# Kernel optimization log

Hardware: AMD Instinct MI355X
Metric: run time of the kernel (lower is better)

The kernel has to match this reference:

```python
import jax, jax.numpy as jnp
import numpy as np
from jax import lax

B, LEN_SEQ, D_MODEL, N_HEAD, FACTOR, D_FF = 16, 512, 512, 8, 5, 2048
EPS = 1e-5


def layer_norm(x):
    mu = x.mean(-1, keepdims=True)
    var = ((x - mu) ** 2).mean(-1, keepdims=True)
    return (x - mu) * lax.rsqrt(var + EPS)


def pos_encode(x):
    pos = jnp.arange(LEN_SEQ, dtype=jnp.float32)[:, None]
    div = jnp.exp(jnp.arange(0, D_MODEL, 2, dtype=jnp.float32) * (-np.log(10000.0) / D_MODEL))
    pe = jnp.zeros((LEN_SEQ, D_MODEL))
    pe = pe.at[:, 0::2].set(jnp.sin(pos * div)).at[:, 1::2].set(jnp.cos(pos * div))
    return x + pe[None]


def prob_attention(Q, K, V, rkey):
    # Q,K,V: [B,H,L,D]; Informer ProbSparse attention, mask_flag=False
    Bq, H, L_Q, D = Q.shape
    L_K = K.shape[2]
    U_part = min(FACTOR * int(np.ceil(np.log(L_K))), L_K)   # sampled keys per query
    u = min(FACTOR * int(np.ceil(np.log(L_Q))), L_Q)        # top queries kept
    idx = jax.random.randint(rkey, (L_Q, U_part), 0, L_K)
    K_samp = K[:, :, idx, :]                                # [B,H,L_Q,U_part,D]
    QK_samp = jnp.einsum('bhld,bhlsd->bhls', Q, K_samp)
    M = QK_samp.max(-1) - QK_samp.sum(-1) / L_K             # sparsity measure
    _, top = lax.top_k(M, u)                                # [B,H,u]
    Q_red = jnp.take_along_axis(Q, top[..., None], axis=2)  # [B,H,u,D]
    scores = jnp.einsum('bhud,bhkd->bhuk', Q_red, K) * (1.0 / np.sqrt(D))
    upd = jnp.einsum('bhuk,bhkd->bhud', jax.nn.softmax(scores, -1), V)
    ctx = jnp.broadcast_to(V.mean(2, keepdims=True), (Bq, H, L_Q, D))
    bi = jnp.arange(Bq)[:, None, None]
    hi = jnp.arange(H)[None, :, None]
    return ctx.at[bi, hi, top].set(upd)


def setup_inputs():
    key = jax.random.key(0)
    ks = jax.random.split(key, 12)
    s = 0.02
    d, f = D_MODEL, D_FF
    n = jax.random.normal
    return {
        'input_data': n(ks[0], (B, LEN_SEQ, d), jnp.float32),
        'Wq': n(ks[1], (d, d)) * s, 'bq': jnp.zeros((d,)),
        'Wk': n(ks[2], (d, d)) * s, 'bk': jnp.zeros((d,)),
        'Wv': n(ks[3], (d, d)) * s, 'bv': jnp.zeros((d,)),
        'Wo': n(ks[4], (d, d)) * s, 'bo': jnp.zeros((d,)),
        'enc_w1': n(ks[5], (d, f)) * s, 'enc_b1': jnp.zeros((f,)),
        'enc_w2': n(ks[6], (f, d)) * s, 'enc_b2': jnp.zeros((d,)),
        'dec_w1': n(ks[7], (d, f)) * s, 'dec_b1': jnp.zeros((f,)),
        'dec_w2': n(ks[8], (f, d)) * s, 'dec_b2': jnp.zeros((d,)),
        'dist_w': n(ks[9], (d, d, 3)) * s, 'dist_b': jnp.zeros((d,)),
        'out_w': n(ks[10], (d, 1)) * s, 'out_b': jnp.zeros((1,)),
    }


def reference(input_data, Wq, bq, Wk, bk, Wv, bv, Wo, bo,
              enc_w1, enc_b1, enc_w2, enc_b2,
              dec_w1, dec_b1, dec_w2, dec_b2,
              dist_w, dist_b, out_w, out_b):
    base = jax.random.key(42)

    def attn(q_in, k_in, v_in, i):
        Bq, L, _ = q_in.shape
        S = k_in.shape[1]
        Q = (q_in @ Wq + bq).reshape(Bq, L, N_HEAD, -1).transpose(0, 2, 1, 3)
        K = (k_in @ Wk + bk).reshape(Bq, S, N_HEAD, -1).transpose(0, 2, 1, 3)
        V = (v_in @ Wv + bv).reshape(Bq, S, N_HEAD, -1).transpose(0, 2, 1, 3)
        ctx = prob_attention(Q, K, V, jax.random.fold_in(base, i))
        return ctx.transpose(0, 2, 1, 3).reshape(Bq, L, -1) @ Wo + bo

    def encoder(x, i):
        x = layer_norm(x + attn(x, x, x, i))
        y = jax.nn.relu(x @ enc_w1 + enc_b1) @ enc_w2 + enc_b2
        return layer_norm(x + y)

    def distill(x):  # conv1d(circular) + batchnorm + ELU + maxpool(3,2,1)
        xc = x.transpose(0, 2, 1)                                   # [B,d,L]
        xp = jnp.concatenate([xc[..., -1:], xc, xc[..., :1]], -1)   # circular pad
        y = lax.conv_general_dilated(xp, dist_w, (1,), 'VALID',
                                     dimension_numbers=('NCH', 'OIH', 'NCH'))
        y = y + dist_b[None, :, None]
        mu = y.mean((0, 2), keepdims=True)
        var = ((y - mu) ** 2).mean((0, 2), keepdims=True)
        y = jax.nn.elu((y - mu) * lax.rsqrt(var + EPS))
        y = lax.reduce_window(y, -jnp.inf, lax.max, (1, 1, 3), (1, 1, 2),
                              [(0, 0), (0, 0), (1, 1)])
        return y.transpose(0, 2, 1)

    enc_inp = pos_encode(input_data)
    dec_inp = pos_encode(input_data)
    e = distill(encoder(enc_inp, 0))   # 512 -> 256
    e = distill(encoder(e, 1))         # 256 -> 128
    e = distill(encoder(e, 2))         # 128 -> 64
    # decoder (source DecoderLayer never applies its norms; dropout = identity in eval)
    out1 = dec_inp + attn(dec_inp, dec_inp, dec_inp, 3)
    out2 = out1 + attn(out1, e, e, 4)
    y = jax.nn.relu(out2 @ dec_w1 + dec_b1) @ dec_w2 + dec_b2
    out3 = y + out2
    return out3 @ out_w + out_b
```

## Files before the change

### kernel.cpp

```cpp
#include <hip/hip_runtime.h>
#include <cstdint>
#include <cmath>


#define HD __host__ __device__

typedef short short8 __attribute__((ext_vector_type(8)));
typedef float float4v __attribute__((ext_vector_type(4)));

__device__ inline short f2bf(float f) {
    unsigned u = __float_as_uint(f);
    unsigned r = u + 0x7FFFu + ((u >> 16) & 1u);
    return (short)(r >> 16);
}

HD inline unsigned rotl32(unsigned x, int r) { return (x << r) | (x >> (32 - r)); }
HD inline void tfround(unsigned& x0, unsigned& x1, int r) {
    x0 += x1; x1 = rotl32(x1, r); x1 ^= x0;
}
HD inline void threefry2x32(unsigned k0, unsigned k1, unsigned c0, unsigned c1,
                            unsigned& o0, unsigned& o1) {
    unsigned ks2 = k0 ^ k1 ^ 0x1BD11BDAu;
    unsigned x0 = c0 + k0, x1 = c1 + k1;
    tfround(x0, x1, 13); tfround(x0, x1, 15); tfround(x0, x1, 26); tfround(x0, x1, 6);
    x0 += k1; x1 += ks2 + 1u;
    tfround(x0, x1, 17); tfround(x0, x1, 29); tfround(x0, x1, 16); tfround(x0, x1, 24);
    x0 += ks2; x1 += k0 + 2u;
    tfround(x0, x1, 13); tfround(x0, x1, 15); tfround(x0, x1, 26); tfround(x0, x1, 6);
    x0 += k0; x1 += k1 + 3u;
    tfround(x0, x1, 17); tfround(x0, x1, 29); tfround(x0, x1, 16); tfround(x0, x1, 24);
    x0 += k1; x1 += ks2 + 4u;
    tfround(x0, x1, 13); tfround(x0, x1, 15); tfround(x0, x1, 26); tfround(x0, x1, 6);
    x0 += ks2; x1 += k0 + 5u;
    o0 = x0; o1 = x1;
}


__global__ void pe_add_k(const float* __restrict__ in, float* __restrict__ out,
                         short* __restrict__ outb, int total) {
    int t = blockIdx.x * 256 + threadIdx.x;
    if (t >= total) return;
    int d = t % 512;
    int l = (t / 512) % 512;
    float i2 = (float)(d & ~1);
    float div = expf(i2 * (-0.017988946039016f));
    float ang = (float)l * div;
    float v = (d & 1) ? cosf(ang) : sinf(ang);
    float r = in[t] + v;
    out[t] = r;
    outb[t] = f2bf(r);
}

__global__ __launch_bounds__(256) void transpose_bf16_k(const float* __restrict__ in,
                                                        short* __restrict__ out, int K, int N) {
    __shared__ float tile[32][33];
    int k0 = blockIdx.y * 32, n0 = blockIdx.x * 32;
    int c = threadIdx.x & 31, r0 = threadIdx.x >> 5;
    for (int rr = r0; rr < 32; rr += 8)
        tile[rr][c] = in[(size_t)(k0 + rr) * N + n0 + c];
    __syncthreads();
    for (int rr = r0; rr < 32; rr += 8)
        out[(size_t)(n0 + rr) * K + k0 + c] = f2bf(tile[c][rr]);
}

__global__ void w2t_k(const float* __restrict__ dw, short* __restrict__ out, int total) {
    int t = blockIdx.x * 256 + threadIdx.x;
    if (t >= total) return;
    int kk = t % 1536;
    int o = t / 1536;
    int h = kk / 512, i = kk % 512;
    out[t] = f2bf(dw[(size_t)o * 1536 + i * 3 + h]);
}

__global__ void bcat_k(const float* __restrict__ b0, const float* __restrict__ b1,
                       const float* __restrict__ b2, float* __restrict__ out) {
    int t = blockIdx.x * 256 + threadIdx.x;
    if (t >= 1536) return;
    out[t] = (t < 512) ? b0[t] : (t < 1024 ? b1[t - 512] : b2[t - 1024]);
}

__device__ inline void swizzle_bid(int bid, int nbx, int nby, int& bm, int& bn) {
    if ((nby & 7) == 0) {
        int stripe = nby >> 3;
        int x = bid & 7, w = bid >> 3;
        bn = w % nbx;
        bm = x * stripe + w / nbx;
    } else {
        bn = bid % nbx;
        bm = bid / nbx;
    }
}

__global__ __launch_bounds__(256) void gemm128_k(
    const short* __restrict__ A, const short* __restrict__ Bt,
    const float* __restrict__ bias, const float* __restrict__ res,
    float* __restrict__ C32, short* __restrict__ C16,
    int M, int N, int K, int relu, int ldC) {
    __shared__ short As[128 * 40];
    __shared__ short Bs[128 * 40];
    int tid = threadIdx.x;
    int wave = tid >> 6, lane = tid & 63;
    int wy = wave >> 1, wx = wave & 1;
    int rl = lane & 15, quad = lane >> 4;
    int bm, bn;
    swizzle_bid(blockIdx.x, N >> 7, M >> 7, bm, bn);
    bm <<= 7; bn <<= 7;

    float4v acc[4][4];
    #pragma unroll
    for (int i = 0; i < 4; i++)
        #pragma unroll
        for (int j = 0; j < 4; j++) acc[i][j] = (float4v){0.f, 0.f, 0.f, 0.f};

    for (int k0 = 0; k0 < K; k0 += 32) {
        #pragma unroll
        for (int it = 0; it < 2; it++) {
            int c = tid + it * 256;
            int row = c >> 2, seg = c & 3;
            *(float4*)&As[row * 40 + seg * 8] =
                *(const float4*)(A + (size_t)(bm + row) * K + k0 + seg * 8);
        }
        #pragma unroll
        for (int it = 0; it < 2; it++) {
            int c = tid + it * 256;
            int row = c >> 2, seg = c & 3;
            *(float4*)&Bs[row * 40 + seg * 8] =
                *(const float4*)(Bt + (size_t)(bn + row) * K + k0 + seg * 8);
        }
        __syncthreads();
        short8 a[4], b[4];
        #pragma unroll
        for (int i = 0; i < 4; i++)
            a[i] = *(const short8*)&As[(wy * 64 + i * 16 + rl) * 40 + quad * 8];
        #pragma unroll
        for (int j = 0; j < 4; j++)
            b[j] = *(const short8*)&Bs[(wx * 64 + j * 16 + rl) * 40 + quad * 8];
        #pragma unroll
        for (int i = 0; i < 4; i++)
            #pragma unroll
            for (int j = 0; j < 4; j++)
                acc[i][j] = __builtin_amdgcn_mfma_f32_16x16x32_bf16(a[i], b[j], acc[i][j], 0, 0, 0);
        __syncthreads();
    }
    #pragma unroll
    for (int i = 0; i < 4; i++) {
        #pragma unroll
        for (int r = 0; r < 4; r++) {
            int gm = bm + wy * 64 + i * 16 + quad * 4 + r;
            #pragma unroll
            for (int j = 0; j < 4; j++) {
                int gn = bn + wx * 64 + j * 16 + rl;
                float v = acc[i][j][r];
                if (bias) v += bias[gn];
                if (relu) v = fmaxf(v, 0.f);
                if (res) v += res[(size_t)gm * ldC + gn];
                if (C32) C32[(size_t)gm * ldC + gn] = v;
                if (C16) C16[(size_t)gm * ldC + gn] = f2bf(v);
            }
        }
    }
}

__global__ __launch_bounds__(256) void gemm64_k(
    const short* __restrict__ A, const short* __restrict__ Bt,
    const float* __restrict__ bias, const float* __restrict__ res,
    float* __restrict__ C32, short* __restrict__ C16,
    int M, int N, int K, int relu, int ldC) {
    __shared__ short As[64 * 40];
    __shared__ short Bs[64 * 40];
    int tid = threadIdx.x;
    int wave = tid >> 6, lane = tid & 63;
    int rl = lane & 15, quad = lane >> 4;
    int bm, bn;
    swizzle_bid(blockIdx.x, N >> 6, M >> 6, bm, bn);
    bm <<= 6; bn <<= 6;

    float4v acc[4];
    #pragma unroll
    for (int j = 0; j < 4; j++) acc[j] = (float4v){0.f, 0.f, 0.f, 0.f};

    int row = tid >> 2, seg = tid & 3;
    for (int k0 = 0; k0 < K; k0 += 32) {
        *(float4*)&As[row * 40 + seg * 8] =
            *(const float4*)(A + (size_t)(bm + row) * K + k0 + seg * 8);
        *(float4*)&Bs[row * 40 + seg * 8] =
            *(const float4*)(Bt + (size_t)(bn + row) * K + k0 + seg * 8);
        __syncthreads();
        short8 a = *(const short8*)&As[(wave * 16 + rl) * 40 + quad * 8];
        short8 b[4];
        #pragma unroll
        for (int j = 0; j < 4; j++)
            b[j] = *(const short8*)&Bs[(j * 16 + rl) * 40 + quad * 8];
        #pragma unroll
        for (int j = 0; j < 4; j++)
            acc[j] = __builtin_amdgcn_mfma_f32_16x16x32_bf16(a, b[j], acc[j], 0, 0, 0);
        __syncthreads();
    }
    #pragma unroll
    for (int r = 0; r < 4; r++) {
        int gm = bm + wave * 16 + quad * 4 + r;
        #pragma unroll
        for (int j = 0; j < 4; j++) {
            int gn = bn + j * 16 + rl;
            float v = acc[j][r];
            if (bias) v += bias[gn];
            if (relu) v = fmaxf(v, 0.f);
            if (res) v += res[(size_t)gm * ldC + gn];
            if (C32) C32[(size_t)gm * ldC + gn] = v;
            if (C16) C16[(size_t)gm * ldC + gn] = f2bf(v);
        }
    }
}

__global__ void ridx_k(unsigned k0, unsigned k1, int size, unsigned mask, int* __restrict__ idx) {
    int j = blockIdx.x * 256 + threadIdx.x;
    if (j >= size) return;
    unsigned o0, o1;
    threefry2x32(k0, k1, (unsigned)j, (unsigned)(j + size), o0, o1);
    idx[j] = (int)(o1 & mask);
}

extern __shared__ float kslab[];
__global__ __launch_bounds__(256) void msamp_lds_k(
    const float* __restrict__ Qp, const float* __restrict__ Kp,
    const int* __restrict__ idx, float* __restrict__ Mout,
    int LQ, int LK, int U, int ld) {
    int bid = blockIdx.x;
    int half = bid & 1;
    int bh = bid >> 1;
    int h = bh & 7, b = bh >> 3;
    const float* kbase = Kp + (size_t)b * LK * ld + h * 64;
    for (int t = threadIdx.x; t < LK * 16; t += 256) {
        int r = t >> 4, seg = t & 15;
        float4 v = *(const float4*)(kbase + (size_t)r * ld + seg * 4);
        float* dst = &kslab[r * 65 + seg * 4];
        dst[0] = v.x; dst[1] = v.y; dst[2] = v.z; dst[3] = v.w;
    }
    __syncthreads();
    int halfL = LQ >> 1;
    for (int li = threadIdx.x; li < halfL; li += 256) {
        int l = half * halfL + li;
        const float4* q = (const float4*)(Qp + (size_t)(b * LQ + l) * ld + h * 64);
        float qr[64];
        #pragma unroll
        for (int d4 = 0; d4 < 16; d4++) {
            float4 v = q[d4];
            qr[4 * d4] = v.x; qr[4 * d4 + 1] = v.y; qr[4 * d4 + 2] = v.z; qr[4 * d4 + 3] = v.w;
        }
        const int* ip = idx + l * U;
        float mx = -INFINITY, sm = 0.f;
        for (int s = 0; s < U; s++) {
            const float* kr = &kslab[ip[s] * 65];
            float acc = 0.f;
            #pragma unroll
            for (int d = 0; d < 64; d++) acc += qr[d] * kr[d];
            mx = fmaxf(mx, acc);
            sm += acc;
        }
        Mout[(size_t)bh * LQ + l] = mx - sm / (float)LK;
    }
}

__global__ void msamp_k(const float* __restrict__ Qp, const float* __restrict__ Kp,
                        const int* __restrict__ idx, float* __restrict__ Mout,
                        int LQ, int LK, int U, int ld) {
    int t = blockIdx.x * 256 + threadIdx.x;
    int total = 16 * 8 * LQ * 4;
    if (t >= total) return;
    int p = t & 3;
    int rest = t >> 2;
    int l = rest % LQ;
    int h = (rest / LQ) & 7;
    int b = rest / (LQ * 8);
    const float4* q = (const float4*)(Qp + ((size_t)(b * LQ + l) * ld + h * 64));
    const float* kb = Kp + ((size_t)b * LK * ld + h * 64);
    float4 qr[16];
    #pragma unroll
    for (int d = 0; d < 16; d++) qr[d] = q[d];
    float mx = -INFINITY, sm = 0.f;
    for (int s = p; s < U; s += 4) {
        const float4* kr = (const float4*)(kb + (size_t)idx[l * U + s] * ld);
        float acc = 0.f;
        #pragma unroll
        for (int d = 0; d < 16; d++) {
            float4 kv = kr[d];
            acc += qr[d].x * kv.x + qr[d].y * kv.y + qr[d].z * kv.z + qr[d].w * kv.w;
        }
        mx = fmaxf(mx, acc);
        sm += acc;
    }
    mx = fmaxf(mx, __shfl_xor(mx, 1));
    mx = fmaxf(mx, __shfl_xor(mx, 2));
    sm += __shfl_xor(sm, 1);
    sm += __shfl_xor(sm, 2);
    if (p == 0)
        Mout[(size_t)((b * 8) + h) * LQ + l] = mx - sm / (float)LK;
}

__global__ __launch_bounds__(256) void topk_k(const float* __restrict__ M,
                                              int* __restrict__ top, int LQ, int u) {
    __shared__ float vals[512];
    __shared__ float rv[256];
    __shared__ int ri[256];
    int bh = blockIdx.x;
    int tid = threadIdx.x;
    const float* m = M + (size_t)bh * LQ;
    for (int l = tid; l < LQ; l += 256) vals[l] = m[l];
    __syncthreads();
    for (int j = 0; j < u; j++) {
        float best = -INFINITY;
        int bi = LQ;
        for (int l = tid; l < LQ; l += 256) {
            float v = vals[l];
            if (v > best) { best = v; bi = l; }
        }
        rv[tid] = best; ri[tid] = bi;
        __syncthreads();
        for (int s = 128; s > 0; s >>= 1) {
            if (tid < s) {
                float v2 = rv[tid + s]; int i2 = ri[tid + s];
                if (v2 > rv[tid] || (v2 == rv[tid] && i2 < ri[tid])) { rv[tid] = v2; ri[tid] = i2; }
            }
            __syncthreads();
        }
        int sel = ri[0];
        if (tid == 0) {
            top[bh * u + j] = sel;
            vals[sel] = -INFINITY;
        }
        __syncthreads();
    }
}

__global__ __launch_bounds__(256) void vmean_k(const float* __restrict__ Vp,
                                               float* __restrict__ vm, int LK, int ld) {
    __shared__ float red[8][33];
    int b = blockIdx.y;
    int c0 = blockIdx.x * 32;
    int ci = threadIdx.x & 31, g = threadIdx.x >> 5;
    const float* base = Vp + (size_t)b * LK * ld + c0 + ci;
    float s = 0.f;
    for (int l = g; l < LK; l += 8) s += base[(size_t)l * ld];
    red[g][ci] = s;
    __syncthreads();
    if (threadIdx.x < 32) {
        float t = 0.f;
        #pragma unroll
        for (int g2 = 0; g2 < 8; g2++) t += red[g2][threadIdx.x];
        vm[b * 512 + c0 + threadIdx.x] = t / (float)LK;
    }
}

__global__ void ctx_fill_k(const float* __restrict__ vm, short* __restrict__ ctxb,
                           int LQ, int total) {
    int t = blockIdx.x * 256 + threadIdx.x;
    if (t >= total) return;
    int c = t % 512;
    int b = t / (512 * LQ);
    ctxb[t] = f2bf(vm[b * 512 + c]);
}

__global__ __launch_bounds__(256) void attn_flash_k(
    const float* __restrict__ Qp, const float* __restrict__ Kp, const float* __restrict__ Vp,
    const int* __restrict__ top, short* __restrict__ ctxb, int LQ, int LK, int u, int ld) {
    __shared__ float qs[18][64];
    __shared__ int ls[18];
    __shared__ float kv[64][65];
    __shared__ float sc[18][512];
    int bid = blockIdx.x;
    int chunk = bid & 1;
    int h = (bid >> 1) & 7;
    int b = bid >> 4;
    int CH = (u + 1) >> 1;
    int r0 = chunk * CH;
    int nr = min(CH, u - r0);
    int tid = threadIdx.x;
    int wave = tid >> 6, lane = tid & 63;

    if (tid < nr) ls[tid] = top[((b * 8) + h) * u + r0 + tid];
    __syncthreads();
    for (int t = tid; t < nr * 16; t += 256) {
        int r = t >> 4, seg = t & 15;
        float4 v = *(const float4*)(Qp + ((size_t)(b * LQ + ls[r])) * ld + h * 64 + seg * 4);
        float* dst = &qs[r][seg * 4];
        dst[0] = v.x; dst[1] = v.y; dst[2] = v.z; dst[3] = v.w;
    }

    int ntile = LK >> 6;
    const float* kbase = Kp + ((size_t)b * LK) * ld + h * 64;
    for (int T = 0; T < ntile; T++) {
        __syncthreads();
        #pragma unroll
        for (int it = 0; it < 4; it++) {
            int t = tid + it * 256;
            int kk = t >> 4, seg = t & 15;
            float4 v = *(const float4*)(kbase + (size_t)(T * 64 + kk) * ld + seg * 4);
            float* dst = &kv[kk][seg * 4];
            dst[0] = v.x; dst[1] = v.y; dst[2] = v.z; dst[3] = v.w;
        }
        __syncthreads();
        for (int p = tid; p < nr * 64; p += 256) {
            int r = p >> 6, kk = p & 63;
            float acc = 0.f;
            #pragma unroll
            for (int d = 0; d < 64; d++) acc += qs[r][d] * kv[kk][d];
            sc[r][T * 64 + kk] = acc * 0.125f;
        }
    }
    __syncthreads();
    for (int r = wave; r < nr; r += 4) {
        float mx = -INFINITY;
        for (int k = lane; k < LK; k += 64) mx = fmaxf(mx, sc[r][k]);
        #pragma unroll
        for (int o = 32; o > 0; o >>= 1) mx = fmaxf(mx, __shfl_xor(mx, o));
        float s = 0.f;
        for (int k = lane; k < LK; k += 64) {
            float e = expf(sc[r][k] - mx);
            sc[r][k] = e;
            s += e;
        }
        #pragma unroll
        for (int o = 32; o > 0; o >>= 1) s += __shfl_xor(s, o);
        float inv = 1.0f / s;
        for (int k = lane; k < LK; k += 64) sc[r][k] *= inv;
    }
    float acc[5];
    #pragma unroll
    for (int i = 0; i < 5; i++) acc[i] = 0.f;
    const float* vbase = Vp + ((size_t)b * LK) * ld + h * 64;
    for (int T = 0; T < ntile; T++) {
        __syncthreads();
        #pragma unroll
        for (int it = 0; it < 4; it++) {
            int t = tid + it * 256;
            int kk = t >> 4, seg = t & 15;
            float4 v = *(const float4*)(vbase + (size_t)(T * 64 + kk) * ld + seg * 4);
            float* dst = &kv[kk][seg * 4];
            dst[0] = v.x; dst[1] = v.y; dst[2] = v.z; dst[3] = v.w;
        }
        __syncthreads();
        int ri = 0;
        for (int r = wave; r < nr; r += 4, ri++) {
            float a = 0.f;
            #pragma unroll
            for (int kk = 0; kk < 64; kk++) a += sc[r][T * 64 + kk] * kv[kk][lane];
            acc[ri] += a;
        }
    }
    int ri = 0;
    for (int r = wave; r < nr; r += 4, ri++)
        ctxb[((size_t)(b * LQ + ls[r])) * 512 + h * 64 + lane] = f2bf(acc[ri]);
}

__global__ __launch_bounds__(256) void ln_k(const float* __restrict__ in,
                                            float* __restrict__ out, short* __restrict__ outb) {
    __shared__ float red[256];
    int r = blockIdx.x;
    int tid = threadIdx.x;
    const float* x = in + (size_t)r * 512;
    float a = x[tid], b = x[tid + 256];
    red[tid] = a + b;
    __syncthreads();
    for (int s = 128; s > 0; s >>= 1) {
        if (tid < s) red[tid] += red[tid + s];
        __syncthreads();
    }
    float mu = red[0] / 512.f;
    __syncthreads();
    float d1 = a - mu, d2 = b - mu;
    red[tid] = d1 * d1 + d2 * d2;
    __syncthreads();
    for (int s = 128; s > 0; s >>= 1) {
        if (tid < s) red[tid] += red[tid + s];
        __syncthreads();
    }
    float inv = 1.0f / sqrtf(red[0] / 512.f + 1e-5f);
    float v1 = d1 * inv, v2 = d2 * inv;
    out[(size_t)r * 512 + tid] = v1;
    out[(size_t)r * 512 + tid + 256] = v2;
    if (outb) {
        outb[(size_t)r * 512 + tid] = f2bf(v1);
        outb[(size_t)r * 512 + tid + 256] = f2bf(v2);
    }
}

__global__ void xcat_k(const float* __restrict__ x, short* __restrict__ xc, int L, int total) {
    int t = blockIdx.x * 256 + threadIdx.x;
    if (t >= total) return;
    int i = t % 512;
    int h = (t / 512) % 3;
    int bt = t / 1536;
    int tt = bt % L;
    int b = bt / L;
    int src = (tt + h - 1 + L) % L;
    xc[t] = f2bf(x[(size_t)(b * L + src) * 512 + i]);
}

__global__ __launch_bounds__(256) void bnstats_k(const float* __restrict__ y,
                                                 float* __restrict__ mu, float* __restrict__ var,
                                                 int rows) {
    __shared__ float red[256];
    int o = blockIdx.x;
    int tid = threadIdx.x;
    float s = 0.f;
    for (int r = tid; r < rows; r += 256) s += y[(size_t)r * 512 + o];
    red[tid] = s;
    __syncthreads();
    for (int st = 128; st > 0; st >>= 1) {
        if (tid < st) red[tid] += red[tid + st];
        __syncthreads();
    }
    float m = red[0] / (float)rows;
    __syncthreads();
    float s2 = 0.f;
    for (int r = tid; r < rows; r += 256) {
        float d = y[(size_t)r * 512 + o] - m;
        s2 += d * d;
    }
    red[tid] = s2;
    __syncthreads();
    for (int st = 128; st > 0; st >>= 1) {
        if (tid < st) red[tid] += red[tid + st];
        __syncthreads();
    }
    if (tid == 0) {
        mu[o] = m;
        var[o] = red[0] / (float)rows;
    }
}

__global__ void elu_pool_k(const float* __restrict__ y, const float* __restrict__ mu,
                           const float* __restrict__ var, float* __restrict__ out,
                           short* __restrict__ outb, int L, int total) {
    int t = blockIdx.x * 256 + threadIdx.x;
    if (t >= total) return;
    int o = t % 512;
    int tp = (t / 512) % (L / 2);
    int b = t / (512 * (L / 2));
    float mm = mu[o];
    float inv = 1.0f / sqrtf(var[o] + 1e-5f);
    float m = -INFINITY;
    #pragma unroll
    for (int dt = 0; dt < 3; dt++) {
        int tt = 2 * tp - 1 + dt;
        if (tt < 0 || tt >= L) continue;
        float v = (y[(size_t)(b * L + tt) * 512 + o] - mm) * inv;
        m = fmaxf(m, v);
    }
    float r = m > 0.f ? m : expm1f(m);
    out[t] = r;
    outb[t] = f2bf(r);
}

__global__ void final_k(const float* __restrict__ x, const float* __restrict__ w,
                        const float* __restrict__ bb, float* __restrict__ out, int rows) {
    int gid = blockIdx.x * 256 + threadIdx.x;
    int wid = gid >> 6;
    int lane = gid & 63;
    if (wid >= rows) return;
    const float* xr = x + (size_t)wid * 512;
    float acc = 0.f;
    for (int k = lane; k < 512; k += 64) acc += xr[k] * w[k];
    for (int off = 32; off > 0; off >>= 1) acc += __shfl_down(acc, off);
    if (lane == 0) out[wid] = acc + bb[0];
}


static inline int iceil_log(int L) { return (int)ceil(log((double)L)); }
static inline int imin(int a, int b) { return a < b ? a : b; }

extern "C" void kernel_launch(void* const* d_in, const int* in_sizes, int n_in,
                              void* d_out, int out_size, void* d_ws, size_t ws_size,
                              hipStream_t stream) {
    const float* IN  = (const float*)d_in[0];
    const float* Wq  = (const float*)d_in[1];
    const float* bq  = (const float*)d_in[2];
    const float* Wk  = (const float*)d_in[3];
    const float* bk  = (const float*)d_in[4];
    const float* Wv  = (const float*)d_in[5];
    const float* bv  = (const float*)d_in[6];
    const float* Wo  = (const float*)d_in[7];
    const float* bo  = (const float*)d_in[8];
    const float* ew1 = (const float*)d_in[9];
    const float* eb1 = (const float*)d_in[10];
    const float* ew2 = (const float*)d_in[11];
    const float* eb2 = (const float*)d_in[12];
    const float* dw1 = (const float*)d_in[13];
    const float* db1 = (const float*)d_in[14];
    const float* dw2 = (const float*)d_in[15];
    const float* db2 = (const float*)d_in[16];
    const float* DW  = (const float*)d_in[17];
    const float* db  = (const float*)d_in[18];
    const float* ow  = (const float*)d_in[19];
    const float* ob  = (const float*)d_in[20];
    float* OUT = (float*)d_out;

    float* ws = (float*)d_ws;
    size_t off = 0;
    auto alloc = [&](size_t n) { float* p = ws + off; off += n; return p; };
    float* PE   = alloc(4194304);
    short* PEb  = (short*)alloc(2097152);
    float* QKV  = alloc(12582912);
    float* CTX  = alloc(4194304);
    short* CTXb = (short*)alloc(2097152);
    float* T1   = alloc(4194304);
    short* T1b  = (short*)alloc(2097152);
    float* XLN  = alloc(4194304);
    short* XLNb = (short*)alloc(2097152);
    float* T2   = alloc(4194304);
    short* T2b  = (short*)alloc(2097152);
    float* T3   = alloc(4194304);
    short* HIDb = (short*)alloc(8388608);
    float* D1   = alloc(2097152);
    short* D1b  = (short*)alloc(1048576);
    float* D2   = alloc(1048576);
    short* D2b  = (short*)alloc(524288);
    short* Ebb  = (short*)alloc(262144);
    float* Ebf  = alloc(524288);
    float* MB   = alloc(65536);
    float* VM   = alloc(8192);
    float* MU   = alloc(512);
    float* VARb = alloc(512);
    float* BQKV = alloc(1536);
    int* IDX  = (int*)alloc(17920);
    int* TOPB = (int*)alloc(4480);
    short* WqkvT = (short*)alloc(393216);
    short* WoT   = (short*)alloc(131072);
    short* ew1T  = (short*)alloc(524288);
    short* ew2T  = (short*)alloc(524288);
    short* dw1T  = (short*)alloc(524288);
    short* dw2T  = (short*)alloc(524288);
    short* W2T   = (short*)alloc(393216);
    (void)ws_size; (void)n_in; (void)in_sizes; (void)out_size;

    static_assert(512 * 65 * 4 == 133120, "");
    hipError_t attr_ok = hipFuncSetAttribute(
        (const void*)msamp_lds_k, hipFuncAttributeMaxDynamicSharedMemorySize, 133120);

    auto gemm128 = [&](const short* A, const short* Bt, const float* bias, const float* res,
                       float* C32, short* C16, int M, int N, int K, int relu, int ldC) {
        gemm128_k<<<(N / 128) * (M / 128), 256, 0, stream>>>(A, Bt, bias, res, C32, C16,
                                                             M, N, K, relu, ldC);
    };
    auto gemm64 = [&](const short* A, const short* Bt, const float* bias, const float* res,
                      float* C32, short* C16, int M, int N, int K, int relu, int ldC) {
        gemm64_k<<<(N / 64) * (M / 64), 256, 0, stream>>>(A, Bt, bias, res, C32, C16,
                                                          M, N, K, relu, ldC);
    };
    auto tr = [&](const float* W, short* Wt, int K, int N) {
        dim3 g(N / 32, K / 32);
        transpose_bf16_k<<<g, 256, 0, stream>>>(W, Wt, K, N);
    };

    auto attn = [&](const short* qinb, const short* kvinb, const float* resp,
                    float* out32, short* out16, int LQ, int LK, int ikey) {
        int Mq = 16 * LQ, Mk = 16 * LK;
        const int ld = 1536;
        float* Qp = QKV;
        float* Kp = QKV + 512;
        float* Vp = QKV + 1024;
        if (qinb == kvinb) {
            gemm128(qinb, WqkvT, BQKV, nullptr, QKV, nullptr, Mq, 1536, 512, 0, ld);
        } else {
            gemm64(qinb, WqkvT, BQKV, nullptr, QKV, nullptr, Mq, 512, 512, 0, ld);
            gemm64(kvinb, WqkvT + 512 * 512, BQKV + 512, nullptr, QKV + 512, nullptr,
                   Mk, 1024, 512, 0, ld);
        }
        int U = imin(5 * iceil_log(LK), LK);
        int u = imin(5 * iceil_log(LQ), LQ);
        unsigned rk0, rk1;
        threefry2x32(0u, 42u, 0u, (unsigned)ikey, rk0, rk1);
        int size = LQ * U;
        ridx_k<<<(size + 255) / 256, 256, 0, stream>>>(rk0, rk1, size, (unsigned)(LK - 1), IDX);
        size_t shbytes = (size_t)LK * 65 * 4;
        if (attr_ok == hipSuccess || shbytes <= 65536) {
            msamp_lds_k<<<16 * 8 * 2, 256, shbytes, stream>>>(Qp, Kp, IDX, MB, LQ, LK, U, ld);
        } else {
            int totM = 16 * 8 * LQ * 4;
            msamp_k<<<(totM + 255) / 256, 256, 0, stream>>>(Qp, Kp, IDX, MB, LQ, LK, U, ld);
        }
        topk_k<<<128, 256, 0, stream>>>(MB, TOPB, LQ, u);
        vmean_k<<<dim3(16, 16), 256, 0, stream>>>(Vp, VM, LK, ld);
        int totC = 16 * LQ * 512;
        ctx_fill_k<<<(totC + 255) / 256, 256, 0, stream>>>(VM, CTXb, LQ, totC);
        attn_flash_k<<<16 * 8 * 2, 256, 0, stream>>>(Qp, Kp, Vp, TOPB, CTXb, LQ, LK, u, ld);
        gemm64(CTXb, WoT, bo, resp, out32, out16, Mq, 512, 512, 0, 512);
    };

    auto encoder = [&](const short* Xb, const float* X, int L, int ikey, float* OUTenc) {
        int M = 16 * L;
        attn(Xb, Xb, X, T1, nullptr, L, L, ikey);
        ln_k<<<M, 256, 0, stream>>>(T1, XLN, XLNb);
        gemm128(XLNb, ew1T, eb1, nullptr, nullptr, HIDb, M, 2048, 512, 1, 2048);
        gemm64(HIDb, ew2T, eb2, XLN, T2, nullptr, M, 512, 2048, 0, 512);
        ln_k<<<M, 256, 0, stream>>>(T2, OUTenc, nullptr);
    };

    auto distill = [&](const float* X, int L, float* OUTd, short* OUTdb) {
        int M = 16 * L;
        int tot = M * 1536;
        xcat_k<<<(tot + 255) / 256, 256, 0, stream>>>(X, HIDb, L, tot);
        gemm64(HIDb, W2T, db, nullptr, CTX, nullptr, M, 512, 1536, 0, 512);
        bnstats_k<<<512, 256, 0, stream>>>(CTX, MU, VARb, M);
        int toto = 16 * (L / 2) * 512;
        elu_pool_k<<<(toto + 255) / 256, 256, 0, stream>>>(CTX, MU, VARb, OUTd, OUTdb, L, toto);
    };

    tr(Wq, WqkvT, 512, 512);
    tr(Wk, WqkvT + 512 * 512, 512, 512);
    tr(Wv, WqkvT + 1024 * 512, 512, 512);
    tr(Wo, WoT, 512, 512);
    tr(ew1, ew1T, 512, 2048);
    tr(ew2, ew2T, 2048, 512);
    tr(dw1, dw1T, 512, 2048);
    tr(dw2, dw2T, 2048, 512);
    w2t_k<<<(786432 + 255) / 256, 256, 0, stream>>>(DW, W2T, 786432);
    bcat_k<<<6, 256, 0, stream>>>(bq, bk, bv, BQKV);

    int totPE = 16 * 512 * 512;
    pe_add_k<<<(totPE + 255) / 256, 256, 0, stream>>>(IN, PE, PEb, totPE);

    encoder(PEb, PE, 512, 0, T3); distill(T3, 512, D1, D1b);
    encoder(D1b, D1, 256, 1, T3); distill(T3, 256, D2, D2b);
    encoder(D2b, D2, 128, 2, T3); distill(T3, 128, Ebf, Ebb);

    attn(PEb, PEb, PE, T1, T1b, 512, 512, 3);
    attn(T1b, Ebb, T1, T2, T2b, 512, 64, 4);
    gemm128(T2b, dw1T, db1, nullptr, nullptr, HIDb, 8192, 2048, 512, 1, 2048);
    gemm64(HIDb, dw2T, db2, T2, T3, nullptr, 8192, 512, 2048, 0, 512);
    final_k<<<(8192 * 64) / 256, 256, 0, stream>>>(T3, ow, ob, OUT, 8192);
}
```

Measured before the change: 1.653 ms.

## Replace strided per-channel batchnorm stats with coalesced two-stage partial reduction

The old stats kernel had one block per channel reading a column with a stride of 512 floats, and it made two passes, one for the mean and one for the variance. The new version has 128 blocks that each read contiguous row chunks in a coalesced way and accumulate the sum and sum of squares in a single pass. A small second kernel then combines the partials into the mean and the variance. This cuts uncoalesced memory traffic and the number of passes, at the cost of computing variance as E[x^2]-m^2, which is less numerically stable, and one extra launch.

```diff
diff --git a/kernel.cpp b/kernel.cpp
--- a/kernel.cpp
+++ b/kernel.cpp
@@ -496,37 +496,38 @@
     xc[t] = f2bf(x[(size_t)(b * L + src) * 512 + i]);
 }
 
-__global__ __launch_bounds__(256) void bnstats_k(const float* __restrict__ y,
-                                                 float* __restrict__ mu, float* __restrict__ var,
-                                                 int rows) {
-    __shared__ float red[256];
-    int o = blockIdx.x;
+__global__ __launch_bounds__(256) void bnpart_k(const float* __restrict__ y,
+                                                float* __restrict__ ps, float* __restrict__ pq,
+                                                int rows) {
+    int chunk = blockIdx.x;
+    int rpc = rows >> 7;
+    int r0 = chunk * rpc;
     int tid = threadIdx.x;
-    float s = 0.f;
-    for (int r = tid; r < rows; r += 256) s += y[(size_t)r * 512 + o];
-    red[tid] = s;
-    __syncthreads();
-    for (int st = 128; st > 0; st >>= 1) {
-        if (tid < st) red[tid] += red[tid + st];
-        __syncthreads();
-    }
-    float m = red[0] / (float)rows;
-    __syncthreads();
-    float s2 = 0.f;
-    for (int r = tid; r < rows; r += 256) {
-        float d = y[(size_t)r * 512 + o] - m;
-        s2 += d * d;
-    }
-    red[tid] = s2;
-    __syncthreads();
-    for (int st = 128; st > 0; st >>= 1) {
-        if (tid < st) red[tid] += red[tid + st];
-        __syncthreads();
-    }
-    if (tid == 0) {
-        mu[o] = m;
-        var[o] = red[0] / (float)rows;
-    }
+    float s0 = 0.f, s1 = 0.f, q0 = 0.f, q1 = 0.f;
+    for (int r = r0; r < r0 + rpc; r++) {
+        float a = y[(size_t)r * 512 + tid];
+        float b = y[(size_t)r * 512 + tid + 256];
+        s0 += a; q0 += a * a;
+        s1 += b; q1 += b * b;
+    }
+    ps[chunk * 512 + tid] = s0;
+    ps[chunk * 512 + tid + 256] = s1;
+    pq[chunk * 512 + tid] = q0;
+    pq[chunk * 512 + tid + 256] = q1;
+}
+
+__global__ void bnfin_k(const float* __restrict__ ps, const float* __restrict__ pq,
+                        float* __restrict__ mu, float* __restrict__ var, int rows) {
+    int o = blockIdx.x * 256 + threadIdx.x;
+    if (o >= 512) return;
+    float s = 0.f, q = 0.f;
+    for (int c = 0; c < 128; c++) {
+        s += ps[c * 512 + o];
+        q += pq[c * 512 + o];
+    }
+    float m = s / (float)rows;
+    mu[o] = m;
+    var[o] = q / (float)rows - m * m;
 }
 
 __global__ void elu_pool_k(const float* __restrict__ y, const float* __restrict__ mu,
@@ -622,6 +623,8 @@
     float* MU   = alloc(512);
     float* VARb = alloc(512);
     float* BQKV = alloc(1536);
+    float* PS   = alloc(65536);
+    float* PQ   = alloc(65536);
     int* IDX  = (int*)alloc(17920);
     int* TOPB = (int*)alloc(4480);
     short* WqkvT = (short*)alloc(393216);
@@ -701,7 +704,8 @@
         int tot = M * 1536;
         xcat_k<<<(tot + 255) / 256, 256, 0, stream>>>(X, HIDb, L, tot);
         gemm64(HIDb, W2T, db, nullptr, CTX, nullptr, M, 512, 1536, 0, 512);
-        bnstats_k<<<512, 256, 0, stream>>>(CTX, MU, VARb, M);
+        bnpart_k<<<128, 256, 0, stream>>>(CTX, PS, PQ, M);
+        bnfin_k<<<2, 256, 0, stream>>>(PS, PQ, MU, VARb, M);
         int toto = 16 * (L / 2) * 512;
         elu_pool_k<<<(toto + 255) / 256, 256, 0, stream>>>(CTX, MU, VARb, OUTd, OUTdb, L, toto);
     };
```

After: 1.611 ms (median of 2 runs). 2.5% less time.
